# Kernel tuning notes

Hardware: AMD Instinct MI355X
Metric: run time of the kernel (lower is better)

Reference implementation:

```python
import jax, jax.numpy as jnp
import numpy as np

B, T, SDR, D, H = 2, 1024, 2048, 1024, 16
DH = D // H
FFN_H = int(D * 4.0 * 2 / 3)  # SwiGLU 2/3 rule -> 2730
N_FHN_STEPS = 4
FHN_DT = 0.1
FHN_A = 0.7
FHN_B = 0.8
FHN_TAU = 12.5
FHN_THRESHOLD = 0.5


def _layernorm(x, g, b, eps=1e-5):
    mu = jnp.mean(x, axis=-1, keepdims=True)
    var = jnp.var(x, axis=-1, keepdims=True)
    return (x - mu) * jax.lax.rsqrt(var + eps) * g + b


def setup_inputs() -> dict:
    key = jax.random.key(0)
    ks = jax.random.split(key, 16)
    s = 0.02
    return {
        "sdr": jax.random.normal(ks[0], (B, T, SDR), jnp.float32),
        "sdr_w": jax.random.normal(ks[1], (SDR, D), jnp.float32) * s,
        "sdr_b": jnp.zeros((D,), jnp.float32),
        "w_qkv": jax.random.normal(ks[2], (D, 3 * D), jnp.float32) * s,
        "b_qkv": jnp.zeros((3 * D,), jnp.float32),
        "w_out": jax.random.normal(ks[3], (D, D), jnp.float32) * s,
        "b_out": jnp.zeros((D,), jnp.float32),
        "ln1_g": jnp.ones((D,), jnp.float32),
        "ln1_b": jnp.zeros((D,), jnp.float32),
        "ln2_g": jnp.ones((D,), jnp.float32),
        "ln2_b": jnp.zeros((D,), jnp.float32),
        "w_gate": jax.random.normal(ks[4], (D, FFN_H), jnp.float32) * s,
        "w_up": jax.random.normal(ks[5], (D, FFN_H), jnp.float32) * s,
        "w_down": jax.random.normal(ks[6], (FFN_H, D), jnp.float32) * s,
    }


def _fhn_attention(h, w_qkv, b_qkv, w_out, b_out):
    # h: (B, T, D). Causal MHA whose pre-softmax scores are evolved by
    # FitzHugh-Nagumo soliton dynamics with IMEX (explicit v, implicit w) steps.
    qkv = h @ w_qkv + b_qkv
    q, k, vals = jnp.split(qkv, 3, axis=-1)
    q = q.reshape(B, T, H, DH).transpose(0, 2, 1, 3)      # bhtd
    k = k.reshape(B, T, H, DH).transpose(0, 2, 1, 3)
    vals = vals.reshape(B, T, H, DH).transpose(0, 2, 1, 3)
    scores = jnp.einsum("bhqd,bhkd->bhqk", q, k) / jnp.sqrt(jnp.float32(DH))
    # FHN IMEX integration: v' = v - v^3/3 - w + I ; tau w' = v + a - b w
    v = scores
    w = jnp.zeros_like(scores)
    w_denom = 1.0 + FHN_DT * FHN_B / FHN_TAU
    for _ in range(N_FHN_STEPS):
        v = v + FHN_DT * (v - v * v * v / 3.0 - w + scores)  # explicit
        w = (w + FHN_DT * (v + FHN_A) / FHN_TAU) / w_denom   # implicit linear
    logits = v - FHN_THRESHOLD
    causal = jnp.tril(jnp.ones((T, T), bool))
    logits = jnp.where(causal, logits, -1e9)
    attn = jax.nn.softmax(logits, axis=-1)
    ctx = jnp.einsum("bhqk,bhkd->bhqd", attn, vals)
    ctx = ctx.transpose(0, 2, 1, 3).reshape(B, T, D)
    return ctx @ w_out + b_out


def reference(sdr, sdr_w, sdr_b, w_qkv, b_qkv, w_out, b_out,
              ln1_g, ln1_b, ln2_g, ln2_b, w_gate, w_up, w_down):
    x = sdr @ sdr_w + sdr_b                                   # sdr_proj
    attn_out = _fhn_attention(_layernorm(x, ln1_g, ln1_b),
                              w_qkv, b_qkv, w_out, b_out)
    x = x + attn_out                                          # residual
    h2 = _layernorm(x, ln2_g, ln2_b)
    mlp = (jax.nn.silu(h2 @ w_gate) * (h2 @ w_up)) @ w_down   # SwiGLU
    return x + mlp
```

## Files before the change

### kernel.cpp

```cpp
#include <hip/hip_runtime.h>
#include <hip/hip_bf16.h>
#include <math.h>


typedef __bf16 bf16;
typedef __bf16 bf16x4 __attribute__((ext_vector_type(4)));
typedef __bf16 bf16x8 __attribute__((ext_vector_type(8)));
typedef float  f32x4  __attribute__((ext_vector_type(4)));

#define DEV __device__ __forceinline__

DEV void gload_lds16(const void* g, void* l) {
  __builtin_amdgcn_global_load_lds(
      (const __attribute__((address_space(1))) void*)g,
      (__attribute__((address_space(3))) void*)l, 16, 0, 0);
}

__global__ __launch_bounds__(256) void k_convert(const float* __restrict__ in,
                                                 bf16* __restrict__ out, int n) {
  int i = (blockIdx.x * 256 + threadIdx.x) * 4;
  if (i < n) {
    float4 f = *(const float4*)(in + i);
    bf16x4 o;
    o[0] = (bf16)f.x; o[1] = (bf16)f.y; o[2] = (bf16)f.z; o[3] = (bf16)f.w;
    *(bf16x4*)(out + i) = o;
  }
}

__global__ __launch_bounds__(256) void k_transpose_wt(const float* __restrict__ in,
    bf16* __restrict__ out, int K, int N, int Kpad, int Npad) {
  __shared__ float tile[32][33];
  const int kb = blockIdx.x * 32, nb = blockIdx.y * 32;
  const int tx = threadIdx.x & 31, ty = threadIdx.x >> 5;
  for (int i = ty; i < 32; i += 8) {
    int k = kb + i, n = nb + tx;
    tile[i][tx] = (k < K && n < N) ? in[(size_t)k * N + n] : 0.f;
  }
  __syncthreads();
  for (int i = ty; i < 32; i += 8) {
    int n = nb + i, k = kb + tx;
    if (n < Npad && k < Kpad) out[(size_t)n * Kpad + k] = (bf16)tile[tx][i];
  }
}

__global__ __launch_bounds__(256) void k_layernorm(const float* __restrict__ x,
    const float* __restrict__ gw, const float* __restrict__ bw, bf16* __restrict__ out) {
  const int row = blockIdx.x;
  const int t = threadIdx.x;
  const float* xr = x + (size_t)row * 1024;
  float4 f = *(const float4*)(xr + t * 4);
  float s  = f.x + f.y + f.z + f.w;
  float s2 = f.x * f.x + f.y * f.y + f.z * f.z + f.w * f.w;
  #pragma unroll
  for (int o = 32; o > 0; o >>= 1) { s += __shfl_down(s, o, 64); s2 += __shfl_down(s2, o, 64); }
  __shared__ float rA[4], rB[4];
  const int wid = t >> 6;
  if ((t & 63) == 0) { rA[wid] = s; rB[wid] = s2; }
  __syncthreads();
  s  = rA[0] + rA[1] + rA[2] + rA[3];
  s2 = rB[0] + rB[1] + rB[2] + rB[3];
  const float mu   = s * (1.f / 1024.f);
  const float var  = fmaxf(s2 * (1.f / 1024.f) - mu * mu, 0.f);
  const float rstd = rsqrtf(var + 1e-5f);
  float4 g4 = *(const float4*)(gw + t * 4);
  float4 b4 = *(const float4*)(bw + t * 4);
  bf16x4 o4;
  o4[0] = (bf16)((f.x - mu) * rstd * g4.x + b4.x);
  o4[1] = (bf16)((f.y - mu) * rstd * g4.y + b4.y);
  o4[2] = (bf16)((f.z - mu) * rstd * g4.z + b4.z);
  o4[3] = (bf16)((f.w - mu) * rstd * g4.w + b4.w);
  *(bf16x4*)(out + (size_t)row * 1024 + t * 4) = o4;
}

enum { EPI_BIAS = 1, EPI_BIAS_RES = 2, EPI_RES = 3, EPI_QKV = 5 };

template <int EPI>
DEV void gemm_epilogue(int rb, int cc, int Nn, const f32x4& a,
                       float* C, const float* bias, const float* res,
                       bf16* qp, bf16* kp, float* vbuf) {
  float bv = 0.f;
  if constexpr (EPI == EPI_BIAS || EPI == EPI_BIAS_RES || EPI == EPI_QKV) bv = bias[cc];
  #pragma unroll
  for (int v = 0; v < 4; ++v) {
    const int row = rb + v;
    float val = a[v] + bv;
    if constexpr (EPI == EPI_QKV) {
      const int bq = row >> 10, tt = row & 1023;
      if (cc < 1024) {
        qp[(size_t)(bq * 16 + (cc >> 6)) * 65536 + (size_t)tt * 64 + (cc & 63)] = (bf16)(val * 0.125f);
      } else if (cc < 2048) {
        const int c2 = cc - 1024;
        kp[(size_t)(bq * 16 + (c2 >> 6)) * 65536 + (size_t)tt * 64 + (c2 & 63)] = (bf16)val;
      } else {
        vbuf[(size_t)row * 1024 + (cc - 2048)] = val;
      }
    } else {
      const size_t idx = (size_t)row * Nn + cc;
      if constexpr (EPI == EPI_BIAS_RES || EPI == EPI_RES) val += res[idx];
      C[idx] = val;
    }
  }
}

template <int EPI>
__global__ __launch_bounds__(256, 2)
void k_gemm(const bf16* __restrict__ A, const bf16* __restrict__ Bt,
            float* __restrict__ C, const float* __restrict__ bias,
            const float* __restrict__ res, bf16* __restrict__ qp,
            bf16* __restrict__ kp, float* __restrict__ vbuf, int Nn, int Kk) {
  __shared__ __align__(16) bf16 As[2][128 * 64];
  __shared__ __align__(16) bf16 Bs[2][128 * 64];
  const int t = threadIdx.x;
  const int lane = t & 63, wid = t >> 6;
  const int wr = wid >> 1, wc = wid & 1;
  const int row0 = blockIdx.y * 128, col0 = blockIdx.x * 128;
  const int g  = t & 7;
  const int r0 = t >> 3;
  const int c16s = g ^ (r0 & 7);
  f32x4 acc[4][4] = {};

  auto stage = [&](int buf, int k0) {
    #pragma unroll
    for (int it = 0; it < 4; ++it) {
      int r = r0 + it * 32;
      gload_lds16(A + (size_t)(row0 + r) * Kk + k0 + c16s * 8, &As[buf][(it * 256 + wid * 64) * 8]);
    }
    #pragma unroll
    for (int it = 0; it < 4; ++it) {
      int r = r0 + it * 32;
      gload_lds16(Bt + (size_t)(col0 + r) * Kk + k0 + c16s * 8, &Bs[buf][(it * 256 + wid * 64) * 8]);
    }
  };

  stage(0, 0);
  __syncthreads();
  int cur = 0;
  for (int k0 = 0; k0 < Kk; k0 += 64) {
    if (k0 + 64 < Kk) stage(cur ^ 1, k0 + 64);
    #pragma unroll
    for (int ks = 0; ks < 2; ++ks) {
      bf16x8 af[4], bfv[4];
      #pragma unroll
      for (int m = 0; m < 4; ++m) {
        int rr = wr * 64 + m * 16 + (lane & 15);
        int c16 = (ks * 4 + (lane >> 4)) ^ (rr & 7);
        af[m] = *(const bf16x8*)&As[cur][rr * 64 + c16 * 8];
      }
      #pragma unroll
      for (int n = 0; n < 4; ++n) {
        int rr = wc * 64 + n * 16 + (lane & 15);
        int c16 = (ks * 4 + (lane >> 4)) ^ (rr & 7);
        bfv[n] = *(const bf16x8*)&Bs[cur][rr * 64 + c16 * 8];
      }
      #pragma unroll
      for (int m = 0; m < 4; ++m)
        #pragma unroll
        for (int n = 0; n < 4; ++n)
          acc[m][n] = __builtin_amdgcn_mfma_f32_16x16x32_bf16(af[m], bfv[n], acc[m][n], 0, 0, 0);
    }
    __syncthreads();
    cur ^= 1;
  }
  #pragma unroll
  for (int m = 0; m < 4; ++m) {
    const int rb = row0 + wr * 64 + m * 16 + ((lane >> 4) << 2);
    #pragma unroll
    for (int n = 0; n < 4; ++n) {
      const int cc = col0 + wc * 64 + n * 16 + (lane & 15);
      gemm_epilogue<EPI>(rb, cc, Nn, acc[m][n], C, bias, res, qp, kp, vbuf);
    }
  }
}

template <int EPI>
__global__ __launch_bounds__(256, 2)
void k_gemm64(const bf16* __restrict__ A, const bf16* __restrict__ Bt,
              float* __restrict__ C, const float* __restrict__ bias,
              const float* __restrict__ res, int Nn, int Kk) {
  __shared__ __align__(16) bf16 As[2][128 * 64];
  __shared__ __align__(16) bf16 Bs[2][64 * 64];
  const int t = threadIdx.x;
  const int lane = t & 63, wid = t >> 6;
  const int row0 = blockIdx.y * 128, col0 = blockIdx.x * 64;
  const int g  = t & 7;
  const int r0 = t >> 3;
  const int c16s = g ^ (r0 & 7);
  f32x4 acc[2][4] = {};

  auto stage = [&](int buf, int k0) {
    #pragma unroll
    for (int it = 0; it < 4; ++it) {
      int r = r0 + it * 32;
      gload_lds16(A + (size_t)(row0 + r) * Kk + k0 + c16s * 8, &As[buf][(it * 256 + wid * 64) * 8]);
    }
    #pragma unroll
    for (int it = 0; it < 2; ++it) {
      int r = r0 + it * 32;
      gload_lds16(Bt + (size_t)(col0 + r) * Kk + k0 + c16s * 8, &Bs[buf][(it * 256 + wid * 64) * 8]);
    }
  };

  stage(0, 0);
  __syncthreads();
  int cur = 0;
  for (int k0 = 0; k0 < Kk; k0 += 64) {
    if (k0 + 64 < Kk) stage(cur ^ 1, k0 + 64);
    #pragma unroll
    for (int ks = 0; ks < 2; ++ks) {
      bf16x8 af[2], bfv[4];
      #pragma unroll
      for (int m = 0; m < 2; ++m) {
        int rr = wid * 32 + m * 16 + (lane & 15);
        int c16 = (ks * 4 + (lane >> 4)) ^ (rr & 7);
        af[m] = *(const bf16x8*)&As[cur][rr * 64 + c16 * 8];
      }
      #pragma unroll
      for (int n = 0; n < 4; ++n) {
        int rr = n * 16 + (lane & 15);
        int c16 = (ks * 4 + (lane >> 4)) ^ (rr & 7);
        bfv[n] = *(const bf16x8*)&Bs[cur][rr * 64 + c16 * 8];
      }
      #pragma unroll
      for (int m = 0; m < 2; ++m)
        #pragma unroll
        for (int n = 0; n < 4; ++n)
          acc[m][n] = __builtin_amdgcn_mfma_f32_16x16x32_bf16(af[m], bfv[n], acc[m][n], 0, 0, 0);
    }
    __syncthreads();
    cur ^= 1;
  }
  #pragma unroll
  for (int m = 0; m < 2; ++m) {
    const int rb = row0 + wid * 32 + m * 16 + ((lane >> 4) << 2);
    #pragma unroll
    for (int n = 0; n < 4; ++n) {
      const int cc = col0 + n * 16 + (lane & 15);
      gemm_epilogue<EPI>(rb, cc, Nn, acc[m][n], C, bias, res, nullptr, nullptr, nullptr);
    }
  }
}

__global__ __launch_bounds__(256, 2)
void k_gemm_swiglu(const bf16* __restrict__ A, const bf16* __restrict__ Bg,
                   const bf16* __restrict__ Bu, bf16* __restrict__ act,
                   int Nn, int Kk) {
  __shared__ __align__(16) bf16 As[128 * 64];
  __shared__ __align__(16) bf16 Bgs[128 * 64];
  __shared__ __align__(16) bf16 Bus[128 * 64];
  const int t = threadIdx.x;
  const int lane = t & 63, wid = t >> 6;
  const int wr = wid >> 1, wc = wid & 1;
  const int row0 = blockIdx.y * 128, col0 = blockIdx.x * 128;
  const int g  = t & 7;
  const int r0 = t >> 3;
  const int c16s = g ^ (r0 & 7);
  f32x4 ag[4][4] = {}, au[4][4] = {};

  for (int k0 = 0; k0 < Kk; k0 += 64) {
    #pragma unroll
    for (int it = 0; it < 4; ++it) {
      int r = r0 + it * 32;
      gload_lds16(A + (size_t)(row0 + r) * Kk + k0 + c16s * 8, &As[(it * 256 + wid * 64) * 8]);
    }
    #pragma unroll
    for (int it = 0; it < 4; ++it) {
      int r = r0 + it * 32;
      gload_lds16(Bg + (size_t)(col0 + r) * Kk + k0 + c16s * 8, &Bgs[(it * 256 + wid * 64) * 8]);
    }
    #pragma unroll
    for (int it = 0; it < 4; ++it) {
      int r = r0 + it * 32;
      gload_lds16(Bu + (size_t)(col0 + r) * Kk + k0 + c16s * 8, &Bus[(it * 256 + wid * 64) * 8]);
    }
    __syncthreads();
    #pragma unroll
    for (int ks = 0; ks < 2; ++ks) {
      bf16x8 af[4], bg[4], bu[4];
      #pragma unroll
      for (int m = 0; m < 4; ++m) {
        int rr = wr * 64 + m * 16 + (lane & 15);
        int c16 = (ks * 4 + (lane >> 4)) ^ (rr & 7);
        af[m] = *(const bf16x8*)&As[rr * 64 + c16 * 8];
      }
      #pragma unroll
      for (int n = 0; n < 4; ++n) {
        int rr = wc * 64 + n * 16 + (lane & 15);
        int c16 = (ks * 4 + (lane >> 4)) ^ (rr & 7);
        bg[n] = *(const bf16x8*)&Bgs[rr * 64 + c16 * 8];
        bu[n] = *(const bf16x8*)&Bus[rr * 64 + c16 * 8];
      }
      #pragma unroll
      for (int m = 0; m < 4; ++m)
        #pragma unroll
        for (int n = 0; n < 4; ++n) {
          ag[m][n] = __builtin_amdgcn_mfma_f32_16x16x32_bf16(af[m], bg[n], ag[m][n], 0, 0, 0);
          au[m][n] = __builtin_amdgcn_mfma_f32_16x16x32_bf16(af[m], bu[n], au[m][n], 0, 0, 0);
        }
    }
    __syncthreads();
  }
  #pragma unroll
  for (int m = 0; m < 4; ++m) {
    const int rb = row0 + wr * 64 + m * 16 + ((lane >> 4) << 2);
    #pragma unroll
    for (int n = 0; n < 4; ++n) {
      const int cc = col0 + wc * 64 + n * 16 + (lane & 15);
      #pragma unroll
      for (int v = 0; v < 4; ++v) {
        float gt = ag[m][n][v], up = au[m][n][v];
        float sg = gt / (1.f + __expf(-gt));
        act[(size_t)(rb + v) * Nn + cc] = (bf16)(sg * up);
      }
    }
  }
}

__global__ __launch_bounds__(256) void k_transpose_v(const float* __restrict__ vbuf,
                                                     bf16* __restrict__ vT) {
  __shared__ float tile[32][33];
  const int bh = blockIdx.z, b = bh >> 4, h = bh & 15;
  const int t0 = blockIdx.x * 32, d0 = blockIdx.y * 32;
  const int tx = threadIdx.x & 31, ty = threadIdx.x >> 5;
  for (int i = ty; i < 32; i += 8)
    tile[i][tx] = vbuf[(size_t)(b * 1024 + t0 + i) * 1024 + h * 64 + d0 + tx];
  __syncthreads();
  for (int i = ty; i < 32; i += 8)
    vT[(size_t)bh * 65536 + (size_t)(d0 + i) * 1024 + t0 + tx] = (bf16)tile[tx][i];
}

#define FHN_DT 0.1f
#define FHN_A_ 0.7f

__global__ __launch_bounds__(256, 4)
void k_attn(const bf16* __restrict__ q, const bf16* __restrict__ k,
            const bf16* __restrict__ vT, bf16* __restrict__ ctx) {
  __shared__ __align__(16) char smem[16896];
  const int bx = blockIdx.x;
  const int pr = bx >> 5;
  const int bh = bx & 31;
  const int b = bh >> 4, hh = bh & 15;
  const int t = threadIdx.x;
  const int lane = t & 63, wid = t >> 6;
  const int l15 = lane & 15, g4 = lane >> 4;
  bf16* Ps    = (bf16*)smem + wid * 1024;
  float* comb = (float*)smem;
  float* mlb  = (float*)(smem + 16384);
  const bf16* qb = q  + (size_t)bh * 65536;
  const bf16* kb = k  + (size_t)bh * 65536;
  const bf16* vb = vT + (size_t)bh * 65536;
  const float wden = 1.0f / (1.0f + FHN_DT * 0.8f / 12.5f);
  const float dtau = FHN_DT / 12.5f;

  #pragma unroll 1
  for (int ph = 0; ph < 2; ++ph) {
    const int s  = ph ? pr : 63 - pr;
    const int q0 = s * 16;
    bf16x8 qf[2];
    #pragma unroll
    for (int ks = 0; ks < 2; ++ks)
      qf[ks] = *(const bf16x8*)(qb + (size_t)(q0 + l15) * 64 + ks * 32 + g4 * 8);

    f32x4 o[4] = {};
    f32x4 mrow = {-1e30f, -1e30f, -1e30f, -1e30f};
    f32x4 ssum = {0.f, 0.f, 0.f, 0.f};
    const int jn = (q0 >> 6) + 1;

    for (int j = wid; j < jn; j += 4) {
      const int kv0 = j * 64;
      f32x4 sc[4] = {};
      #pragma unroll
      for (int ks = 0; ks < 2; ++ks)
        #pragma unroll
        for (int n = 0; n < 4; ++n) {
          bf16x8 kf = *(const bf16x8*)(kb + (size_t)(kv0 + n * 16 + l15) * 64 + ks * 32 + g4 * 8);
          sc[n] = __builtin_amdgcn_mfma_f32_16x16x32_bf16(qf[ks], kf, sc[n], 0, 0, 0);
        }
      const int rbase = q0 + (g4 << 2);
      #pragma unroll
      for (int n = 0; n < 4; ++n)
        #pragma unroll
        for (int v = 0; v < 4; ++v) {
          float sv = sc[n][v];
          float vv = sv, ww = 0.f;
          #pragma unroll
          for (int st = 0; st < 4; ++st) {
            vv = vv + FHN_DT * (vv - vv * vv * vv * (1.f / 3.f) - ww + sv);
            ww = (ww + dtau * (vv + FHN_A_)) * wden;
          }
          float lg = vv - 0.5f;
          if (j == jn - 1) {
            int kvi = kv0 + n * 16 + l15;
            if (kvi > rbase + v) lg = -1e9f;
          }
          sc[n][v] = lg;
        }
      f32x4 mnew, scl;
      #pragma unroll
      for (int v = 0; v < 4; ++v) {
        float m0 = fmaxf(fmaxf(sc[0][v], sc[1][v]), fmaxf(sc[2][v], sc[3][v]));
        #pragma unroll
        for (int msk = 1; msk < 16; msk <<= 1) m0 = fmaxf(m0, __shfl_xor(m0, msk, 64));
        mnew[v] = fmaxf(mrow[v], m0);
        scl[v] = __expf(mrow[v] - mnew[v]);
      }
      #pragma unroll
      for (int v = 0; v < 4; ++v) {
        float rs = 0.f;
        #pragma unroll
        for (int n = 0; n < 4; ++n) {
          float p = __expf(sc[n][v] - mnew[v]);
          sc[n][v] = p;
          rs += p;
        }
        #pragma unroll
        for (int msk = 1; msk < 16; msk <<= 1) rs += __shfl_xor(rs, msk, 64);
        ssum[v] = ssum[v] * scl[v] + rs;
        mrow[v] = mnew[v];
      }
      #pragma unroll
      for (int n = 0; n < 4; ++n) o[n] *= scl;
      #pragma unroll
      for (int n = 0; n < 4; ++n)
        #pragma unroll
        for (int v = 0; v < 4; ++v) {
          int rr = (g4 << 2) + v;
          int c = n * 16 + l15;
          int c16 = (c >> 3) ^ (rr & 7);
          Ps[rr * 64 + c16 * 8 + (c & 7)] = (bf16)sc[n][v];
        }
      #pragma unroll
      for (int ks = 0; ks < 2; ++ks) {
        int c16 = (ks * 4 + g4) ^ (l15 & 7);
        bf16x8 pa = *(const bf16x8*)&Ps[l15 * 64 + c16 * 8];
        #pragma unroll
        for (int n = 0; n < 4; ++n) {
          bf16x8 vf = *(const bf16x8*)(vb + (size_t)(n * 16 + l15) * 1024 + kv0 + ks * 32 + g4 * 8);
          o[n] = __builtin_amdgcn_mfma_f32_16x16x32_bf16(pa, vf, o[n], 0, 0, 0);
        }
      }
    }
    __syncthreads();
    #pragma unroll
    for (int n = 0; n < 4; ++n)
      #pragma unroll
      for (int v = 0; v < 4; ++v)
        comb[(wid * 16 + (g4 << 2) + v) * 64 + n * 16 + l15] = o[n][v];
    if (l15 == 0) {
      #pragma unroll
      for (int v = 0; v < 4; ++v) {
        mlb[(wid * 16 + (g4 << 2) + v) * 2 + 0] = mrow[v];
        mlb[(wid * 16 + (g4 << 2) + v) * 2 + 1] = ssum[v];
      }
    }
    __syncthreads();
    {
      const int row = t >> 4, dseg = t & 15;
      float m = mlb[row * 2];
      #pragma unroll
      for (int w = 1; w < 4; ++w) m = fmaxf(m, mlb[(w * 16 + row) * 2]);
      float L = 0.f;
      f32x4 a = {0.f, 0.f, 0.f, 0.f};
      #pragma unroll
      for (int w = 0; w < 4; ++w) {
        float f = __expf(mlb[(w * 16 + row) * 2] - m);
        L += f * mlb[(w * 16 + row) * 2 + 1];
        f32x4 c = *(const f32x4*)&comb[(w * 16 + row) * 64 + dseg * 4];
        a += c * f;
      }
      const float inv = 1.f / L;
      bf16x4 o4;
      o4[0] = (bf16)(a[0] * inv); o4[1] = (bf16)(a[1] * inv);
      o4[2] = (bf16)(a[2] * inv); o4[3] = (bf16)(a[3] * inv);
      *(bf16x4*)&ctx[(size_t)(b * 1024 + q0 + row) * 1024 + hh * 64 + dseg * 4] = o4;
    }
    __syncthreads();
  }
}

extern "C" void kernel_launch(void* const* d_in, const int* in_sizes, int n_in,
                              void* d_out, int out_size, void* d_ws, size_t ws_size,
                              hipStream_t stream) {
  (void)in_sizes; (void)n_in; (void)out_size; (void)ws_size;
  const float* sdr    = (const float*)d_in[0];
  const float* sdr_w  = (const float*)d_in[1];
  const float* sdr_b  = (const float*)d_in[2];
  const float* w_qkv  = (const float*)d_in[3];
  const float* b_qkv  = (const float*)d_in[4];
  const float* w_out  = (const float*)d_in[5];
  const float* b_out  = (const float*)d_in[6];
  const float* ln1_g  = (const float*)d_in[7];
  const float* ln1_b  = (const float*)d_in[8];
  const float* ln2_g  = (const float*)d_in[9];
  const float* ln2_b  = (const float*)d_in[10];
  const float* w_gate = (const float*)d_in[11];
  const float* w_up   = (const float*)d_in[12];
  const float* w_down = (const float*)d_in[13];
  float* out = (float*)d_out;

  char* wsb = (char*)d_ws;
  size_t off = 0;
  auto alloc = [&](size_t bytes) -> void* {
    void* p = (void*)(wsb + off);
    off += (bytes + 255) & ~(size_t)255;
    return p;
  };
  bf16* sdr_w_t  = (bf16*)alloc(1024ull * 2048 * 2);
  bf16* w_qkv_t  = (bf16*)alloc(3072ull * 1024 * 2);
  bf16* w_out_t  = (bf16*)alloc(1024ull * 1024 * 2);
  bf16* w_gate_t = (bf16*)alloc(2816ull * 1024 * 2);
  bf16* w_up_t   = (bf16*)alloc(2816ull * 1024 * 2);
  bf16* w_down_t = (bf16*)alloc(1024ull * 2816 * 2);
  bf16* big_bf   = (bf16*)alloc(2048ull * 2816 * 2);
  bf16* sdr_bf   = big_bf;
  bf16* act      = big_bf;
  float* x       = (float*)alloc(2048ull * 1024 * 4);
  bf16*  h       = (bf16*)alloc(2048ull * 1024 * 2);
  float* vbuf    = (float*)alloc(2048ull * 1024 * 4);
  bf16*  qb      = (bf16*)alloc(32ull * 1024 * 64 * 2);
  bf16*  kb      = (bf16*)alloc(32ull * 1024 * 64 * 2);
  bf16*  vT      = (bf16*)alloc(32ull * 1024 * 64 * 2);
  bf16*  ctx     = (bf16*)alloc(2048ull * 1024 * 2);
  float* x2      = (float*)alloc(2048ull * 1024 * 4);

  k_convert<<<4096, 256, 0, stream>>>(sdr, sdr_bf, 4194304);
  k_transpose_wt<<<dim3(64, 32),  256, 0, stream>>>(sdr_w,  sdr_w_t,  2048, 1024, 2048, 1024);
  k_transpose_wt<<<dim3(32, 96),  256, 0, stream>>>(w_qkv,  w_qkv_t,  1024, 3072, 1024, 3072);
  k_transpose_wt<<<dim3(32, 32),  256, 0, stream>>>(w_out,  w_out_t,  1024, 1024, 1024, 1024);
  k_transpose_wt<<<dim3(32, 88),  256, 0, stream>>>(w_gate, w_gate_t, 1024, 2730, 1024, 2816);
  k_transpose_wt<<<dim3(32, 88),  256, 0, stream>>>(w_up,   w_up_t,   1024, 2730, 1024, 2816);
  k_transpose_wt<<<dim3(88, 32),  256, 0, stream>>>(w_down, w_down_t, 2730, 1024, 2816, 1024);

  k_gemm64<EPI_BIAS><<<dim3(16, 16), 256, 0, stream>>>(sdr_bf, sdr_w_t, x, sdr_b, nullptr, 1024, 2048);
  k_layernorm<<<2048, 256, 0, stream>>>(x, ln1_g, ln1_b, h);
  k_gemm<EPI_QKV><<<dim3(24, 16), 256, 0, stream>>>(h, w_qkv_t, nullptr, b_qkv, nullptr, qb, kb, vbuf, 3072, 1024);
  k_transpose_v<<<dim3(32, 2, 32), 256, 0, stream>>>(vbuf, vT);
  k_attn<<<1024, 256, 0, stream>>>(qb, kb, vT, ctx);
  k_gemm64<EPI_BIAS_RES><<<dim3(16, 16), 256, 0, stream>>>(ctx, w_out_t, x2, b_out, x, 1024, 1024);
  k_layernorm<<<2048, 256, 0, stream>>>(x2, ln2_g, ln2_b, h);
  k_gemm_swiglu<<<dim3(22, 16), 256, 0, stream>>>(h, w_gate_t, w_up_t, act, 2816, 1024);
  k_gemm64<EPI_RES><<<dim3(16, 16), 256, 0, stream>>>(act, w_down_t, out, nullptr, x2, 1024, 2816);
}
```

Baseline: 366.2 us.

## Merge weight prep launches into one kernel and split attention blocks per query tile

Replaces the bf16 input conversion and six separate weight transpose launches with a single k_prep kernel. It uses 64x64 tiles, vectorized float4 loads and bf16x8 stores, and dispatches on block index. The attention kernel no longer pairs a long and a short query tile in one block. It launches 2048 blocks, one per 16-row tile, ordered longest first, which cuts launch overhead and gives finer load balancing in exchange for more blocks with uneven work.

```diff
diff --git a/kernel.cpp b/kernel.cpp
--- a/kernel.cpp
+++ b/kernel.cpp
@@ -16,30 +16,64 @@
       (__attribute__((address_space(3))) void*)l, 16, 0, 0);
 }
 
-__global__ __launch_bounds__(256) void k_convert(const float* __restrict__ in,
-                                                 bf16* __restrict__ out, int n) {
-  int i = (blockIdx.x * 256 + threadIdx.x) * 4;
-  if (i < n) {
-    float4 f = *(const float4*)(in + i);
-    bf16x4 o;
-    o[0] = (bf16)f.x; o[1] = (bf16)f.y; o[2] = (bf16)f.z; o[3] = (bf16)f.w;
-    *(bf16x4*)(out + i) = o;
-  }
-}
-
-__global__ __launch_bounds__(256) void k_transpose_wt(const float* __restrict__ in,
-    bf16* __restrict__ out, int K, int N, int Kpad, int Npad) {
-  __shared__ float tile[32][33];
-  const int kb = blockIdx.x * 32, nb = blockIdx.y * 32;
-  const int tx = threadIdx.x & 31, ty = threadIdx.x >> 5;
-  for (int i = ty; i < 32; i += 8) {
-    int k = kb + i, n = nb + tx;
-    tile[i][tx] = (k < K && n < N) ? in[(size_t)k * N + n] : 0.f;
-  }
-  __syncthreads();
-  for (int i = ty; i < 32; i += 8) {
-    int n = nb + i, k = kb + tx;
-    if (n < Npad && k < Kpad) out[(size_t)n * Kpad + k] = (bf16)tile[tx][i];
+struct PrepT { const float* in; bf16* out; int K, N, Kpad, nnb; };
+
+__global__ __launch_bounds__(256)
+void k_prep(const float* __restrict__ sdr, bf16* __restrict__ sdr_bf,
+            const float* __restrict__ sdr_w, const float* __restrict__ w_qkv,
+            const float* __restrict__ w_out, const float* __restrict__ w_gate,
+            const float* __restrict__ w_up, const float* __restrict__ w_down,
+            bf16* __restrict__ sdr_w_t, bf16* __restrict__ w_qkv_t,
+            bf16* __restrict__ w_out_t, bf16* __restrict__ w_gate_t,
+            bf16* __restrict__ w_up_t, bf16* __restrict__ w_down_t) {
+  const int bid = blockIdx.x, t = threadIdx.x;
+  if (bid < 512) {
+    const int base = bid * 8192 + t * 4;
+    #pragma unroll
+    for (int p = 0; p < 8; ++p) {
+      const int i = base + p * 1024;
+      float4 f = *(const float4*)(sdr + i);
+      bf16x4 o;
+      o[0] = (bf16)f.x; o[1] = (bf16)f.y; o[2] = (bf16)f.z; o[3] = (bf16)f.w;
+      *(bf16x4*)(sdr_bf + i) = o;
+    }
+    return;
+  }
+  __shared__ float tile[64][65];
+  const float* in; bf16* out; int K, N, Kpad, nnb, lb;
+  if      (bid < 1024) { in = sdr_w;  out = sdr_w_t;  K = 2048; N = 1024; Kpad = 2048; nnb = 16; lb = bid - 512;  }
+  else if (bid < 1792) { in = w_qkv;  out = w_qkv_t;  K = 1024; N = 3072; Kpad = 1024; nnb = 48; lb = bid - 1024; }
+  else if (bid < 2048) { in = w_out;  out = w_out_t;  K = 1024; N = 1024; Kpad = 1024; nnb = 16; lb = bid - 1792; }
+  else if (bid < 2752) { in = w_gate; out = w_gate_t; K = 1024; N = 2730; Kpad = 1024; nnb = 44; lb = bid - 2048; }
+  else if (bid < 3456) { in = w_up;   out = w_up_t;   K = 1024; N = 2730; Kpad = 1024; nnb = 44; lb = bid - 2752; }
+  else                 { in = w_down; out = w_down_t; K = 2730; N = 1024; Kpad = 2816; nnb = 16; lb = bid - 3456; }
+  const int kb = (lb / nnb) * 64, nb = (lb % nnb) * 64;
+  #pragma unroll
+  for (int i = 0; i < 4; ++i) {
+    const int k = kb + (t >> 4) + i * 16;
+    const int n = nb + (t & 15) * 4;
+    float4 f = {0.f, 0.f, 0.f, 0.f};
+    if (k < K) {
+      if (n + 3 < N) f = *(const float4*)(in + (size_t)k * N + n);
+      else {
+        if (n + 0 < N) f.x = in[(size_t)k * N + n + 0];
+        if (n + 1 < N) f.y = in[(size_t)k * N + n + 1];
+        if (n + 2 < N) f.z = in[(size_t)k * N + n + 2];
+        if (n + 3 < N) f.w = in[(size_t)k * N + n + 3];
+      }
+    }
+    float* tr = &tile[(t >> 4) + i * 16][(t & 15) * 4];
+    tr[0] = f.x; tr[1] = f.y; tr[2] = f.z; tr[3] = f.w;
+  }
+  __syncthreads();
+  #pragma unroll
+  for (int i = 0; i < 2; ++i) {
+    const int n = nb + (t >> 3) + i * 32;
+    const int k = kb + (t & 7) * 8;
+    bf16x8 o;
+    #pragma unroll
+    for (int j = 0; j < 8; ++j) o[j] = (bf16)tile[(t & 7) * 8 + j][(t >> 3) + i * 32];
+    *(bf16x8*)(out + (size_t)n * Kpad + k) = o;
   }
 }
 
@@ -336,12 +370,13 @@
             const bf16* __restrict__ vT, bf16* __restrict__ ctx) {
   __shared__ __align__(16) char smem[16896];
   const int bx = blockIdx.x;
-  const int pr = bx >> 5;
+  const int s  = 63 - (bx >> 5);
   const int bh = bx & 31;
   const int b = bh >> 4, hh = bh & 15;
   const int t = threadIdx.x;
   const int lane = t & 63, wid = t >> 6;
   const int l15 = lane & 15, g4 = lane >> 4;
+  const int q0 = s * 16;
   bf16* Ps    = (bf16*)smem + wid * 1024;
   float* comb = (float*)smem;
   float* mlb  = (float*)(smem + 16384);
@@ -351,129 +386,123 @@
   const float wden = 1.0f / (1.0f + FHN_DT * 0.8f / 12.5f);
   const float dtau = FHN_DT / 12.5f;
 
-  #pragma unroll 1
-  for (int ph = 0; ph < 2; ++ph) {
-    const int s  = ph ? pr : 63 - pr;
-    const int q0 = s * 16;
-    bf16x8 qf[2];
+  bf16x8 qf[2];
+  #pragma unroll
+  for (int ks = 0; ks < 2; ++ks)
+    qf[ks] = *(const bf16x8*)(qb + (size_t)(q0 + l15) * 64 + ks * 32 + g4 * 8);
+
+  f32x4 o[4] = {};
+  f32x4 mrow = {-1e30f, -1e30f, -1e30f, -1e30f};
+  f32x4 ssum = {0.f, 0.f, 0.f, 0.f};
+  const int jn = (q0 >> 6) + 1;
+
+  for (int j = wid; j < jn; j += 4) {
+    const int kv0 = j * 64;
+    f32x4 sc[4] = {};
     #pragma unroll
     for (int ks = 0; ks < 2; ++ks)
-      qf[ks] = *(const bf16x8*)(qb + (size_t)(q0 + l15) * 64 + ks * 32 + g4 * 8);
-
-    f32x4 o[4] = {};
-    f32x4 mrow = {-1e30f, -1e30f, -1e30f, -1e30f};
-    f32x4 ssum = {0.f, 0.f, 0.f, 0.f};
-    const int jn = (q0 >> 6) + 1;
-
-    for (int j = wid; j < jn; j += 4) {
-      const int kv0 = j * 64;
-      f32x4 sc[4] = {};
-      #pragma unroll
-      for (int ks = 0; ks < 2; ++ks)
+      #pragma unroll
+      for (int n = 0; n < 4; ++n) {
+        bf16x8 kf = *(const bf16x8*)(kb + (size_t)(kv0 + n * 16 + l15) * 64 + ks * 32 + g4 * 8);
+        sc[n] = __builtin_amdgcn_mfma_f32_16x16x32_bf16(qf[ks], kf, sc[n], 0, 0, 0);
+      }
+    const int rbase = q0 + (g4 << 2);
+    #pragma unroll
+    for (int n = 0; n < 4; ++n)
+      #pragma unroll
+      for (int v = 0; v < 4; ++v) {
+        float sv = sc[n][v];
+        float vv = sv, ww = 0.f;
         #pragma unroll
-        for (int n = 0; n < 4; ++n) {
-          bf16x8 kf = *(const bf16x8*)(kb + (size_t)(kv0 + n * 16 + l15) * 64 + ks * 32 + g4 * 8);
-          sc[n] = __builtin_amdgcn_mfma_f32_16x16x32_bf16(qf[ks], kf, sc[n], 0, 0, 0);
+        for (int st = 0; st < 4; ++st) {
+          vv = vv + FHN_DT * (vv - vv * vv * vv * (1.f / 3.f) - ww + sv);
+          ww = (ww + dtau * (vv + FHN_A_)) * wden;
         }
-      const int rbase = q0 + (g4 << 2);
-      #pragma unroll
-      for (int n = 0; n < 4; ++n)
-        #pragma unroll
-        for (int v = 0; v < 4; ++v) {
-          float sv = sc[n][v];
-          float vv = sv, ww = 0.f;
-          #pragma unroll
-          for (int st = 0; st < 4; ++st) {
-            vv = vv + FHN_DT * (vv - vv * vv * vv * (1.f / 3.f) - ww + sv);
-            ww = (ww + dtau * (vv + FHN_A_)) * wden;
-          }
-          float lg = vv - 0.5f;
-          if (j == jn - 1) {
-            int kvi = kv0 + n * 16 + l15;
-            if (kvi > rbase + v) lg = -1e9f;
-          }
-          sc[n][v] = lg;
+        float lg = vv - 0.5f;
+        if (j == jn - 1) {
+          int kvi = kv0 + n * 16 + l15;
+          if (kvi > rbase + v) lg = -1e9f;
         }
-      f32x4 mnew, scl;
+        sc[n][v] = lg;
+      }
+    f32x4 mnew, scl;
+    #pragma unroll
+    for (int v = 0; v < 4; ++v) {
+      float m0 = fmaxf(fmaxf(sc[0][v], sc[1][v]), fmaxf(sc[2][v], sc[3][v]));
+      #pragma unroll
+      for (int msk = 1; msk < 16; msk <<= 1) m0 = fmaxf(m0, __shfl_xor(m0, msk, 64));
+      mnew[v] = fmaxf(mrow[v], m0);
+      scl[v] = __expf(mrow[v] - mnew[v]);
+    }
+    #pragma unroll
+    for (int v = 0; v < 4; ++v) {
+      float rs = 0.f;
+      #pragma unroll
+      for (int n = 0; n < 4; ++n) {
+        float p = __expf(sc[n][v] - mnew[v]);
+        sc[n][v] = p;
+        rs += p;
+      }
+      #pragma unroll
+      for (int msk = 1; msk < 16; msk <<= 1) rs += __shfl_xor(rs, msk, 64);
+      ssum[v] = ssum[v] * scl[v] + rs;
+      mrow[v] = mnew[v];
+    }
+    #pragma unroll
+    for (int n = 0; n < 4; ++n) o[n] *= scl;
+    #pragma unroll
+    for (int n = 0; n < 4; ++n)
       #pragma unroll
       for (int v = 0; v < 4; ++v) {
-        float m0 = fmaxf(fmaxf(sc[0][v], sc[1][v]), fmaxf(sc[2][v], sc[3][v]));
-        #pragma unroll
-        for (int msk = 1; msk < 16; msk <<= 1) m0 = fmaxf(m0, __shfl_xor(m0, msk, 64));
-        mnew[v] = fmaxf(mrow[v], m0);
-        scl[v] = __expf(mrow[v] - mnew[v]);
-      }
-      #pragma unroll
-      for (int v = 0; v < 4; ++v) {
-        float rs = 0.f;
-        #pragma unroll
-        for (int n = 0; n < 4; ++n) {
-          float p = __expf(sc[n][v] - mnew[v]);
-          sc[n][v] = p;
-          rs += p;
-        }
-        #pragma unroll
-        for (int msk = 1; msk < 16; msk <<= 1) rs += __shfl_xor(rs, msk, 64);
-        ssum[v] = ssum[v] * scl[v] + rs;
-        mrow[v] = mnew[v];
-      }
-      #pragma unroll
-      for (int n = 0; n < 4; ++n) o[n] *= scl;
-      #pragma unroll
-      for (int n = 0; n < 4; ++n)
-        #pragma unroll
-        for (int v = 0; v < 4; ++v) {
-          int rr = (g4 << 2) + v;
-          int c = n * 16 + l15;
-          int c16 = (c >> 3) ^ (rr & 7);
-          Ps[rr * 64 + c16 * 8 + (c & 7)] = (bf16)sc[n][v];
-        }
-      #pragma unroll
-      for (int ks = 0; ks < 2; ++ks) {
-        int c16 = (ks * 4 + g4) ^ (l15 & 7);
-        bf16x8 pa = *(const bf16x8*)&Ps[l15 * 64 + c16 * 8];
-        #pragma unroll
-        for (int n = 0; n < 4; ++n) {
-          bf16x8 vf = *(const bf16x8*)(vb + (size_t)(n * 16 + l15) * 1024 + kv0 + ks * 32 + g4 * 8);
-          o[n] = __builtin_amdgcn_mfma_f32_16x16x32_bf16(pa, vf, o[n], 0, 0, 0);
-        }
-      }
-    }
-    __syncthreads();
-    #pragma unroll
-    for (int n = 0; n < 4; ++n)
-      #pragma unroll
-      for (int v = 0; v < 4; ++v)
-        comb[(wid * 16 + (g4 << 2) + v) * 64 + n * 16 + l15] = o[n][v];
-    if (l15 == 0) {
-      #pragma unroll
-      for (int v = 0; v < 4; ++v) {
-        mlb[(wid * 16 + (g4 << 2) + v) * 2 + 0] = mrow[v];
-        mlb[(wid * 16 + (g4 << 2) + v) * 2 + 1] = ssum[v];
-      }
-    }
-    __syncthreads();
-    {
-      const int row = t >> 4, dseg = t & 15;
-      float m = mlb[row * 2];
-      #pragma unroll
-      for (int w = 1; w < 4; ++w) m = fmaxf(m, mlb[(w * 16 + row) * 2]);
-      float L = 0.f;
-      f32x4 a = {0.f, 0.f, 0.f, 0.f};
-      #pragma unroll
-      for (int w = 0; w < 4; ++w) {
-        float f = __expf(mlb[(w * 16 + row) * 2] - m);
-        L += f * mlb[(w * 16 + row) * 2 + 1];
-        f32x4 c = *(const f32x4*)&comb[(w * 16 + row) * 64 + dseg * 4];
-        a += c * f;
-      }
-      const float inv = 1.f / L;
-      bf16x4 o4;
-      o4[0] = (bf16)(a[0] * inv); o4[1] = (bf16)(a[1] * inv);
-      o4[2] = (bf16)(a[2] * inv); o4[3] = (bf16)(a[3] * inv);
-      *(bf16x4*)&ctx[(size_t)(b * 1024 + q0 + row) * 1024 + hh * 64 + dseg * 4] = o4;
-    }
-    __syncthreads();
+        int rr = (g4 << 2) + v;
+        int c = n * 16 + l15;
+        int c16 = (c >> 3) ^ (rr & 7);
+        Ps[rr * 64 + c16 * 8 + (c & 7)] = (bf16)sc[n][v];
+      }
+    #pragma unroll
+    for (int ks = 0; ks < 2; ++ks) {
+      int c16 = (ks * 4 + g4) ^ (l15 & 7);
+      bf16x8 pa = *(const bf16x8*)&Ps[l15 * 64 + c16 * 8];
+      #pragma unroll
+      for (int n = 0; n < 4; ++n) {
+        bf16x8 vf = *(const bf16x8*)(vb + (size_t)(n * 16 + l15) * 1024 + kv0 + ks * 32 + g4 * 8);
+        o[n] = __builtin_amdgcn_mfma_f32_16x16x32_bf16(pa, vf, o[n], 0, 0, 0);
+      }
+    }
+  }
+  __syncthreads();
+  #pragma unroll
+  for (int n = 0; n < 4; ++n)
+    #pragma unroll
+    for (int v = 0; v < 4; ++v)
+      comb[(wid * 16 + (g4 << 2) + v) * 64 + n * 16 + l15] = o[n][v];
+  if (l15 == 0) {
+    #pragma unroll
+    for (int v = 0; v < 4; ++v) {
+      mlb[(wid * 16 + (g4 << 2) + v) * 2 + 0] = mrow[v];
+      mlb[(wid * 16 + (g4 << 2) + v) * 2 + 1] = ssum[v];
+    }
+  }
+  __syncthreads();
+  {
+    const int row = t >> 4, dseg = t & 15;
+    float m = mlb[row * 2];
+    #pragma unroll
+    for (int w = 1; w < 4; ++w) m = fmaxf(m, mlb[(w * 16 + row) * 2]);
+    float L = 0.f;
+    f32x4 a = {0.f, 0.f, 0.f, 0.f};
+    #pragma unroll
+    for (int w = 0; w < 4; ++w) {
+      float f = __expf(mlb[(w * 16 + row) * 2] - m);
+      L += f * mlb[(w * 16 + row) * 2 + 1];
+      f32x4 c = *(const f32x4*)&comb[(w * 16 + row) * 64 + dseg * 4];
+      a += c * f;
+    }
+    const float inv = 1.f / L;
+    bf16x4 o4;
+    o4[0] = (bf16)(a[0] * inv); o4[1] = (bf16)(a[1] * inv);
+    o4[2] = (bf16)(a[2] * inv); o4[3] = (bf16)(a[3] * inv);
+    *(bf16x4*)&ctx[(size_t)(b * 1024 + q0 + row) * 1024 + hh * 64 + dseg * 4] = o4;
   }
 }
 
@@ -522,19 +551,15 @@
   bf16*  ctx     = (bf16*)alloc(2048ull * 1024 * 2);
   float* x2      = (float*)alloc(2048ull * 1024 * 4);
 
-  k_convert<<<4096, 256, 0, stream>>>(sdr, sdr_bf, 4194304);
-  k_transpose_wt<<<dim3(64, 32),  256, 0, stream>>>(sdr_w,  sdr_w_t,  2048, 1024, 2048, 1024);
-  k_transpose_wt<<<dim3(32, 96),  256, 0, stream>>>(w_qkv,  w_qkv_t,  1024, 3072, 1024, 3072);
-  k_transpose_wt<<<dim3(32, 32),  256, 0, stream>>>(w_out,  w_out_t,  1024, 1024, 1024, 1024);
-  k_transpose_wt<<<dim3(32, 88),  256, 0, stream>>>(w_gate, w_gate_t, 1024, 2730, 1024, 2816);
-  k_transpose_wt<<<dim3(32, 88),  256, 0, stream>>>(w_up,   w_up_t,   1024, 2730, 1024, 2816);
-  k_transpose_wt<<<dim3(88, 32),  256, 0, stream>>>(w_down, w_down_t, 2730, 1024, 2816, 1024);
+  k_prep<<<4160, 256, 0, stream>>>(sdr, sdr_bf, sdr_w, w_qkv, w_out, w_gate,
+                                   w_up, w_down, sdr_w_t, w_qkv_t, w_out_t,
+                                   w_gate_t, w_up_t, w_down_t);
 
   k_gemm64<EPI_BIAS><<<dim3(16, 16), 256, 0, stream>>>(sdr_bf, sdr_w_t, x, sdr_b, nullptr, 1024, 2048);
   k_layernorm<<<2048, 256, 0, stream>>>(x, ln1_g, ln1_b, h);
   k_gemm<EPI_QKV><<<dim3(24, 16), 256, 0, stream>>>(h, w_qkv_t, nullptr, b_qkv, nullptr, qb, kb, vbuf, 3072, 1024);
   k_transpose_v<<<dim3(32, 2, 32), 256, 0, stream>>>(vbuf, vT);
-  k_attn<<<1024, 256, 0, stream>>>(qb, kb, vT, ctx);
+  k_attn<<<2048, 256, 0, stream>>>(qb, kb, vT, ctx);
   k_gemm64<EPI_BIAS_RES><<<dim3(16, 16), 256, 0, stream>>>(ctx, w_out_t, x2, b_out, x, 1024, 1024);
   k_layernorm<<<2048, 256, 0, stream>>>(x2, ln2_g, ln2_b, h);
   k_gemm_swiglu<<<dim3(22, 16), 256, 0, stream>>>(h, w_gate_t, w_up_t, act, 2816, 1024);
```

New measurement: 328.1 us. -10.4%, faster.
